# Optimization experiments

Hardware: AMD Instinct MI355X
Metric: run time of the kernel (lower is better)

Reference implementation:

```python
import jax, jax.numpy as jnp
import numpy as np

D_EMB = 1024
N_HEADS = 16
HEAD_SIZE = 64
LN_EPS = 1e-5


def _layernorm(x, g, b):
    mu = jnp.mean(x, axis=-1, keepdims=True)
    var = jnp.var(x, axis=-1, keepdims=True)
    return (x - mu) * jax.lax.rsqrt(var + LN_EPS) * g + b


def setup_inputs() -> dict:
    key = jax.random.key(0)
    ks = jax.random.split(key, 16)
    B, N, D, H, HS = 8, 1024, D_EMB, N_HEADS, HEAD_SIZE
    s_in = 1.0 / np.sqrt(D)
    s_h = 1.0 / np.sqrt(H * HS)
    s_ff = 1.0 / np.sqrt(4 * D)
    return {
        "x": jax.random.normal(ks[0], (B, N, D), jnp.float32),
        # per-head q/k/v projections, stacked over heads: [H, D, HS]
        "Wq": jax.random.normal(ks[1], (H, D, HS), jnp.float32) * s_in,
        "bq": jnp.zeros((H, HS), jnp.float32),
        "Wk": jax.random.normal(ks[2], (H, D, HS), jnp.float32) * s_in,
        "bk": jnp.zeros((H, HS), jnp.float32),
        "Wv": jax.random.normal(ks[3], (H, D, HS), jnp.float32) * s_in,
        "bv": jnp.zeros((H, HS), jnp.float32),
        "Wproj": jax.random.normal(ks[4], (H * HS, D), jnp.float32) * s_h,
        "bproj": jnp.zeros((D,), jnp.float32),
        "W1": jax.random.normal(ks[5], (D, 4 * D), jnp.float32) * s_in,
        "b1": jnp.zeros((4 * D,), jnp.float32),
        "W2": jax.random.normal(ks[6], (4 * D, D), jnp.float32) * s_ff,
        "b2": jnp.zeros((D,), jnp.float32),
        "ln1_g": jnp.ones((D,), jnp.float32),
        "ln1_b": jnp.zeros((D,), jnp.float32),
        "ln2_g": jnp.ones((D,), jnp.float32),
        "ln2_b": jnp.zeros((D,), jnp.float32),
    }


def reference(x, Wq, bq, Wk, bk, Wv, bv, Wproj, bproj, W1, b1, W2, b2,
              ln1_g, ln1_b, ln2_g, ln2_b):
    # --- pre-LN multi-head attention (dropout = identity in eval) ---
    h = _layernorm(x, ln1_g, ln1_b)                    # [B, N, D]
    q = jnp.einsum('bnd,hds->bhns', h, Wq) + bq[None, :, None, :]
    k = jnp.einsum('bnd,hds->bhns', h, Wk) + bk[None, :, None, :]
    v = jnp.einsum('bnd,hds->bhns', h, Wv) + bv[None, :, None, :]
    scale = 1.0 / jnp.sqrt(jnp.float32(HEAD_SIZE))
    wei = jnp.einsum('bhns,bhms->bhnm', q, k) * scale  # [B, H, N, N]
    wei = jax.nn.softmax(wei, axis=-1)
    attn = jnp.einsum('bhnm,bhms->bhns', wei, v)       # [B, H, N, HS]
    B, H, N, HS = attn.shape
    attn = attn.transpose(0, 2, 1, 3).reshape(B, N, H * HS)  # concat heads
    x = x + attn @ Wproj + bproj
    # --- pre-LN feed-forward with LeakyReLU ---
    h2 = _layernorm(x, ln2_g, ln2_b)
    ff = jax.nn.leaky_relu(h2 @ W1 + b1, negative_slope=0.01) @ W2 + b2
    return x + ff
```

## Files before the change

kernel.cpp:

```cpp
#include <hip/hip_runtime.h>
#include <cstdint>
#include <cstddef>

typedef unsigned short u16;
typedef __attribute__((ext_vector_type(4))) float f32x4;
typedef __attribute__((ext_vector_type(8))) short s16x8;

#define D_EMB 1024
#define NSEQ 1024
#define NB 8
#define NH 16
#define HS 64
#define DFF 4096
#define MTOT (NB*NSEQ)

__device__ __forceinline__ u16 f2bf(float f){
  unsigned u = __float_as_uint(f);
  u += 0x7FFFu + ((u >> 16) & 1u);
  return (u16)(u >> 16);
}

__global__ void transpose_cvt(const float* __restrict__ in, u16* __restrict__ out,
                              int R, int C, size_t inStride, size_t outStride){
  __shared__ float t[32][33];
  const float* ip = in + (size_t)blockIdx.z * inStride;
  u16* op = out + (size_t)blockIdx.z * outStride;
  int c0 = blockIdx.x * 32, r0 = blockIdx.y * 32;
  int tx = threadIdx.x, ty = threadIdx.y;
#pragma unroll
  for (int j = 0; j < 32; j += 8)
    t[ty + j][tx] = ip[(size_t)(r0 + ty + j) * C + (c0 + tx)];
  __syncthreads();
#pragma unroll
  for (int j = 0; j < 32; j += 8)
    op[(size_t)(c0 + ty + j) * R + (r0 + tx)] = f2bf(t[tx][ty + j]);
}

__global__ __launch_bounds__(256) void ln_kernel(const float* __restrict__ x,
    const float* __restrict__ g, const float* __restrict__ bb, u16* __restrict__ out){
  int row = blockIdx.x;
  const float* xr = x + (size_t)row * D_EMB;
  int c = threadIdx.x * 4;
  f32x4 v = *(const f32x4*)(xr + c);
  float s1 = v[0] + v[1] + v[2] + v[3];
  float s2 = v[0]*v[0] + v[1]*v[1] + v[2]*v[2] + v[3]*v[3];
#pragma unroll
  for (int m = 32; m > 0; m >>= 1){ s1 += __shfl_xor(s1, m); s2 += __shfl_xor(s2, m); }
  __shared__ float ps1[4], ps2[4];
  int w = threadIdx.x >> 6;
  if ((threadIdx.x & 63) == 0){ ps1[w] = s1; ps2[w] = s2; }
  __syncthreads();
  s1 = ps1[0] + ps1[1] + ps1[2] + ps1[3];
  s2 = ps2[0] + ps2[1] + ps2[2] + ps2[3];
  float mu = s1 * (1.f / D_EMB);
  float var = s2 * (1.f / D_EMB) - mu * mu;
  float rs = rsqrtf(var + 1e-5f);
  ushort4 o;
  o.x = f2bf((v[0]-mu)*rs*g[c+0] + bb[c+0]);
  o.y = f2bf((v[1]-mu)*rs*g[c+1] + bb[c+1]);
  o.z = f2bf((v[2]-mu)*rs*g[c+2] + bb[c+2]);
  o.w = f2bf((v[3]-mu)*rs*g[c+3] + bb[c+3]);
  *(ushort4*)(out + (size_t)row * D_EMB + c) = o;
}

#define BM 128
#define BN 128
#define BK 32

__device__ __forceinline__ void gload_lds16(const void* g, void* l){
  __builtin_amdgcn_global_load_lds((const __attribute__((address_space(1))) void*)g,
                                   (__attribute__((address_space(3))) void*)l, 16, 0, 0);
}

template<int MODE>
__global__ __launch_bounds__(256) void gemm_bt(
    const u16* __restrict__ A, const u16* __restrict__ Bt,
    int M, int N, int K,
    const float* __restrict__ bias0, const float* __restrict__ bias1,
    const float* __restrict__ bias2, const float* __restrict__ resid,
    void* __restrict__ o0, void* __restrict__ o1, void* __restrict__ o2)
{
  __shared__ alignas(16) u16 Al[2][BM*BK];
  __shared__ alignas(16) u16 Bl[2][BN*BK];
  const int tid = threadIdx.x;
  const int m0 = blockIdx.x * BM, n0 = blockIdx.y * BN;
  const int wid = tid >> 6, lane = tid & 63;
  const int wm = (wid >> 1) * 64, wn = (wid & 1) * 64;
  const int lr = lane & 15, lg = lane >> 4;

  f32x4 zero = {0.f, 0.f, 0.f, 0.f};
  f32x4 acc[4][4];
#pragma unroll
  for (int i = 0; i < 4; i++)
#pragma unroll
    for (int j = 0; j < 4; j++) acc[i][j] = zero;

  const int nk = K / BK;
  const int arow = tid >> 2, akg = tid & 3;

  auto stage = [&](int bufi, int kt){
    const int k0 = kt * BK;
    const u16* ap = A  + (size_t)(m0 + arow) * K + k0 + akg * 8;
    gload_lds16(ap,                  &Al[bufi][tid * 8]);
    gload_lds16(ap + (size_t)64 * K, &Al[bufi][2048 + tid * 8]);
    const u16* bp = Bt + (size_t)(n0 + arow) * K + k0 + akg * 8;
    gload_lds16(bp,                  &Bl[bufi][tid * 8]);
    gload_lds16(bp + (size_t)64 * K, &Bl[bufi][2048 + tid * 8]);
  };

  stage(0, 0);
  for (int kt = 0; kt < nk; ++kt){
    __syncthreads();
    if (kt + 1 < nk) stage((kt + 1) & 1, kt + 1);
    const int bufi = kt & 1;
    s16x8 af[4], bfr[4];
#pragma unroll
    for (int i = 0; i < 4; i++){
      af[i]  = *(const s16x8*)&Al[bufi][(wm + i*16 + lr) * BK + lg * 8];
      bfr[i] = *(const s16x8*)&Bl[bufi][(wn + i*16 + lr) * BK + lg * 8];
    }
#pragma unroll
    for (int i = 0; i < 4; i++)
#pragma unroll
      for (int j = 0; j < 4; j++)
        acc[i][j] = __builtin_amdgcn_mfma_f32_16x16x32_bf16(af[i], bfr[j], acc[i][j], 0, 0, 0);
  }

#pragma unroll
  for (int fm = 0; fm < 4; fm++){
    const int gmb = m0 + wm + fm * 16 + lg * 4;
#pragma unroll
    for (int fn = 0; fn < 4; fn++){
      const int gn = n0 + wn + fn * 16 + lr;
#pragma unroll
      for (int i = 0; i < 4; i++){
        const int gm = gmb + i;
        float v = acc[fm][fn][i];
        if (MODE == 0){
          const int cls = gn >> 10, nn = gn & 1023;
          if (cls == 0)      ((u16*)o0)[(size_t)gm * D_EMB + nn] = f2bf(v + bias0[nn]);
          else if (cls == 1) ((u16*)o1)[(size_t)gm * D_EMB + nn] = f2bf(v + bias1[nn]);
          else {
            const int hh = nn >> 6, ss = nn & 63, bb = gm >> 10, tt = gm & 1023;
            ((u16*)o2)[(((size_t)(bb * NH + hh)) * HS + ss) * NSEQ + tt] = f2bf(v + bias2[nn]);
          }
        } else if (MODE == 1){
          ((float*)o0)[(size_t)gm * N + gn] = resid[(size_t)gm * N + gn] + v + bias0[gn];
        } else {
          float y = v + bias0[gn];
          y = y > 0.f ? y : 0.01f * y;
          ((u16*)o0)[(size_t)gm * N + gn] = f2bf(y);
        }
      }
    }
  }
}

__global__ __launch_bounds__(256) void attn_kernel(
    const u16* __restrict__ Qb, const u16* __restrict__ Kb, const u16* __restrict__ VT,
    u16* __restrict__ attnC)
{
  const int bid = blockIdx.x;
  const int bh = bid & 127, qt = bid >> 7;
  const int b = bh >> 4, h = bh & 15;
  const int tid = threadIdx.x, w = tid >> 6, lane = tid & 63;
  const int lr = lane & 15, lg = lane >> 4;
  const int q0 = qt * 128 + w * 32;

  __shared__ alignas(16) u16 Kl[2][64*64];
  __shared__ alignas(16) u16 Vl[2][64*64];
  __shared__ alignas(16) u16 Pl[4][32][72];

  const int srow = tid >> 3, scg = tid & 7;
  const u16* kbase = Kb + (size_t)(b * NSEQ) * D_EMB + h * HS;
  const u16* vbase = VT + ((size_t)(b * NH + h)) * HS * NSEQ;

  auto stage = [&](int buf, int kt){
    const int tk = kt * 64;
#pragma unroll
    for (int p = 0; p < 2; ++p){
      const int row = srow + p * 32;
      const int sc = scg ^ (row & 7);
      gload_lds16(kbase + (size_t)(tk + row) * D_EMB + sc * 8, &Kl[buf][(p * 256 + tid) * 8]);
      gload_lds16(vbase + (size_t)row * NSEQ + tk + sc * 8,    &Vl[buf][(p * 256 + tid) * 8]);
    }
  };

  s16x8 aq[2][2];
#pragma unroll
  for (int rb = 0; rb < 2; rb++)
#pragma unroll
    for (int kh = 0; kh < 2; kh++)
      aq[rb][kh] = *(const s16x8*)(Qb + (size_t)(b * NSEQ + q0 + rb * 16 + lr) * D_EMB
                                   + h * HS + kh * 32 + lg * 8);

  float m_i[2][4], l_i[2][4];
  f32x4 zero = {0.f, 0.f, 0.f, 0.f};
  f32x4 ao[2][4];
#pragma unroll
  for (int rb = 0; rb < 2; rb++)
#pragma unroll
    for (int i = 0; i < 4; i++){ m_i[rb][i] = -1e30f; l_i[rb][i] = 0.f; ao[rb][i] = zero; }

  const float scale = 0.125f;
  const int rsw = lr & 7;

  stage(0, 0);
  for (int kt = 0; kt < NSEQ / 64; ++kt){
    __syncthreads();
    if (kt + 1 < NSEQ / 64) stage((kt + 1) & 1, kt + 1);
    const int cur = kt & 1;

    f32x4 sv[2][4];
#pragma unroll
    for (int rb = 0; rb < 2; rb++)
#pragma unroll
      for (int fn = 0; fn < 4; fn++) sv[rb][fn] = zero;
#pragma unroll
    for (int fn = 0; fn < 4; fn++){
      const int krow = fn * 16 + lr;
#pragma unroll
      for (int kh = 0; kh < 2; kh++){
        const int chunk = (kh * 4 + lg) ^ rsw;
        s16x8 kf = *(const s16x8*)&Kl[cur][krow * 64 + chunk * 8];
        sv[0][fn] = __builtin_amdgcn_mfma_f32_16x16x32_bf16(aq[0][kh], kf, sv[0][fn], 0, 0, 0);
        sv[1][fn] = __builtin_amdgcn_mfma_f32_16x16x32_bf16(aq[1][kh], kf, sv[1][fn], 0, 0, 0);
      }
    }

#pragma unroll
    for (int rb = 0; rb < 2; rb++){
      float p[4][4];
#pragma unroll
      for (int i = 0; i < 4; i++){
        float s0 = sv[rb][0][i] * scale, s1 = sv[rb][1][i] * scale;
        float s2 = sv[rb][2][i] * scale, s3 = sv[rb][3][i] * scale;
        float rmax = fmaxf(fmaxf(s0, s1), fmaxf(s2, s3));
#pragma unroll
        for (int mm = 8; mm > 0; mm >>= 1) rmax = fmaxf(rmax, __shfl_xor(rmax, mm));
        float mnew = fmaxf(m_i[rb][i], rmax);
        float fac = __expf(m_i[rb][i] - mnew);
        float p0 = __expf(s0 - mnew), p1 = __expf(s1 - mnew);
        float p2 = __expf(s2 - mnew), p3 = __expf(s3 - mnew);
        p[0][i] = p0; p[1][i] = p1; p[2][i] = p2; p[3][i] = p3;
        float rs = (p0 + p1) + (p2 + p3);
#pragma unroll
        for (int mm = 8; mm > 0; mm >>= 1) rs += __shfl_xor(rs, mm);
        l_i[rb][i] = l_i[rb][i] * fac + rs;
        m_i[rb][i] = mnew;
#pragma unroll
        for (int fn = 0; fn < 4; fn++) ao[rb][fn][i] *= fac;
      }
#pragma unroll
      for (int fn = 0; fn < 4; fn++)
#pragma unroll
        for (int i = 0; i < 4; i++)
          Pl[w][rb * 16 + lg * 4 + i][fn * 16 + lr] = f2bf(p[fn][i]);
    }

    s16x8 vf[4][2];
#pragma unroll
    for (int fn = 0; fn < 4; fn++){
      const int vrow = fn * 16 + lr;
#pragma unroll
      for (int kh = 0; kh < 2; kh++){
        const int chunk = (kh * 4 + lg) ^ rsw;
        vf[fn][kh] = *(const s16x8*)&Vl[cur][vrow * 64 + chunk * 8];
      }
    }
#pragma unroll
    for (int rb = 0; rb < 2; rb++){
      s16x8 pa0 = *(const s16x8*)&Pl[w][rb * 16 + lr][lg * 8];
      s16x8 pa1 = *(const s16x8*)&Pl[w][rb * 16 + lr][32 + lg * 8];
#pragma unroll
      for (int fn = 0; fn < 4; fn++){
        ao[rb][fn] = __builtin_amdgcn_mfma_f32_16x16x32_bf16(pa0, vf[fn][0], ao[rb][fn], 0, 0, 0);
        ao[rb][fn] = __builtin_amdgcn_mfma_f32_16x16x32_bf16(pa1, vf[fn][1], ao[rb][fn], 0, 0, 0);
      }
    }
  }

#pragma unroll
  for (int rb = 0; rb < 2; rb++)
#pragma unroll
    for (int fn = 0; fn < 4; fn++)
#pragma unroll
      for (int i = 0; i < 4; i++){
        float v = ao[rb][fn][i] / l_i[rb][i];
        attnC[(size_t)(b * NSEQ + q0 + rb * 16 + lg * 4 + i) * D_EMB + h * HS + fn * 16 + lr] = f2bf(v);
      }
}

extern "C" void kernel_launch(void* const* d_in, const int* in_sizes, int n_in,
                              void* d_out, int out_size, void* d_ws, size_t ws_size,
                              hipStream_t stream)
{
  const float* x    = (const float*)d_in[0];
  const float* Wq   = (const float*)d_in[1];
  const float* bq   = (const float*)d_in[2];
  const float* Wk   = (const float*)d_in[3];
  const float* bk   = (const float*)d_in[4];
  const float* Wv   = (const float*)d_in[5];
  const float* bv   = (const float*)d_in[6];
  const float* Wp   = (const float*)d_in[7];
  const float* bp   = (const float*)d_in[8];
  const float* W1   = (const float*)d_in[9];
  const float* b1   = (const float*)d_in[10];
  const float* W2   = (const float*)d_in[11];
  const float* b2   = (const float*)d_in[12];
  const float* ln1g = (const float*)d_in[13];
  const float* ln1b = (const float*)d_in[14];
  const float* ln2g = (const float*)d_in[15];
  const float* ln2b = (const float*)d_in[16];
  float* out = (float*)d_out;

  char* ws = (char*)d_ws;
  size_t off = 0;
  auto mk = [&](size_t bytes)->void*{ void* p = ws + off; off += (bytes + 255) & ~(size_t)255; return p; };
  u16*  h1    = (u16*) mk((size_t)MTOT * D_EMB * 2);
  u16*  Qb    = (u16*) mk((size_t)MTOT * D_EMB * 2);
  u16*  Kb    = (u16*) mk((size_t)MTOT * D_EMB * 2);
  u16*  VTb   = (u16*) mk((size_t)MTOT * D_EMB * 2);
  u16*  attnC = (u16*) mk((size_t)MTOT * D_EMB * 2);
  float* x1   = (float*)mk((size_t)MTOT * D_EMB * 4);
  u16*  h2    = (u16*) mk((size_t)MTOT * D_EMB * 2);
  u16*  ffb   = (u16*) mk((size_t)MTOT * DFF * 2);
  u16*  WqkvT = (u16*) mk((size_t)3 * D_EMB * D_EMB * 2);
  u16*  WpT   = (u16*) mk((size_t)D_EMB * D_EMB * 2);
  u16*  W1T   = (u16*) mk((size_t)D_EMB * DFF * 2);
  u16*  W2T   = (u16*) mk((size_t)D_EMB * DFF * 2);

  dim3 tb(32, 8, 1);
  transpose_cvt<<<dim3(HS/32, D_EMB/32, NH), tb, 0, stream>>>(Wq, WqkvT,                         D_EMB, HS, (size_t)D_EMB*HS, (size_t)HS*D_EMB);
  transpose_cvt<<<dim3(HS/32, D_EMB/32, NH), tb, 0, stream>>>(Wk, WqkvT + (size_t)D_EMB*D_EMB,   D_EMB, HS, (size_t)D_EMB*HS, (size_t)HS*D_EMB);
  transpose_cvt<<<dim3(HS/32, D_EMB/32, NH), tb, 0, stream>>>(Wv, WqkvT + (size_t)2*D_EMB*D_EMB, D_EMB, HS, (size_t)D_EMB*HS, (size_t)HS*D_EMB);
  transpose_cvt<<<dim3(D_EMB/32, D_EMB/32, 1), tb, 0, stream>>>(Wp, WpT,  D_EMB, D_EMB, 0, 0);
  transpose_cvt<<<dim3(DFF/32,  D_EMB/32, 1), tb, 0, stream>>>(W1, W1T,  D_EMB, DFF,   0, 0);
  transpose_cvt<<<dim3(D_EMB/32, DFF/32,  1), tb, 0, stream>>>(W2, W2T,  DFF,   D_EMB, 0, 0);

  ln_kernel<<<MTOT, 256, 0, stream>>>(x, ln1g, ln1b, h1);

  gemm_bt<0><<<dim3(MTOT/BM, (3*D_EMB)/BN), 256, 0, stream>>>(h1, WqkvT, MTOT, 3*D_EMB, D_EMB,
      bq, bk, bv, nullptr, Qb, Kb, VTb);

  attn_kernel<<<NB*NH*(NSEQ/128), 256, 0, stream>>>(Qb, Kb, VTb, attnC);

  gemm_bt<1><<<dim3(MTOT/BM, D_EMB/BN), 256, 0, stream>>>(attnC, WpT, MTOT, D_EMB, D_EMB,
      bp, nullptr, nullptr, x, x1, nullptr, nullptr);

  ln_kernel<<<MTOT, 256, 0, stream>>>(x1, ln2g, ln2b, h2);

  gemm_bt<2><<<dim3(MTOT/BM, DFF/BN), 256, 0, stream>>>(h2, W1T, MTOT, DFF, D_EMB,
      b1, nullptr, nullptr, nullptr, ffb, nullptr, nullptr);

  gemm_bt<1><<<dim3(MTOT/BM, D_EMB/BN), 256, 0, stream>>>(ffb, W2T, MTOT, D_EMB, DFF,
      b2, nullptr, nullptr, x1, out, nullptr, nullptr);
}
```

Before: 470.9 us.

## Add 256-row 8-wave GEMM with swizzled LDS, XCD remap and split-phase pipelining

Adds a new GEMM kernel with 256xBN tiles, 512 threads, and BK=64 split into two 32-wide halves. It double-buffers through dynamic LDS with an XOR swizzle, interleaves loads with MFMA using barriers and setprio, and remaps block IDs across XCDs. The aim is more data reuse per tile and better overlap of global loads with matrix math for the QKV, projection, FF1 and FF2 GEMMs. The cost is large LDS use (up to 128KB), which limits occupancy, plus a fallback to the old kernel if the shared-memory attribute cannot be set.

```diff
diff --git a/kernel.cpp b/kernel.cpp
--- a/kernel.cpp
+++ b/kernel.cpp
@@ -18,6 +18,11 @@
   unsigned u = __float_as_uint(f);
   u += 0x7FFFu + ((u >> 16) & 1u);
   return (u16)(u >> 16);
+}
+
+__device__ __forceinline__ void gload_lds16(const void* g, void* l){
+  __builtin_amdgcn_global_load_lds((const __attribute__((address_space(1))) void*)g,
+                                   (__attribute__((address_space(3))) void*)l, 16, 0, 0);
 }
 
 __global__ void transpose_cvt(const float* __restrict__ in, u16* __restrict__ out,
@@ -63,15 +68,155 @@
   *(ushort4*)(out + (size_t)row * D_EMB + c) = o;
 }
 
+template<int MODE, int BNT>
+__global__ __launch_bounds__(512) void gemm256(
+    const u16* __restrict__ A, const u16* __restrict__ Bt,
+    int M, int N, int K,
+    const float* __restrict__ bias0, const float* __restrict__ bias1,
+    const float* __restrict__ bias2, const float* __restrict__ resid,
+    void* __restrict__ o0, void* __restrict__ o1, void* __restrict__ o2)
+{
+  constexpr int BMT = 256;
+  constexpr int WCN = BNT/64, WRN = 8/WCN;
+  constexpr int WROWS = BMT/WRN;
+  constexpr int RF = WROWS/16, RH = RF/2;
+  constexpr int ALD = 2, BLD = (BNT*32)/(512*8);
+  constexpr int AHALF = BMT*32, BHALF = BNT*32;
+  extern __shared__ u16 lds[];
+  u16* const Ab = lds;
+  u16* const Bb = lds + 4*AHALF;
+
+  const int tid = threadIdx.x;
+  const int wid = tid>>6, lane = tid&63, lr = lane&15, lg = lane>>4;
+  const int wr = wid/WCN, wc = wid%WCN;
+
+  const int gx = gridDim.x;
+  const int nwg = gx * gridDim.y;
+  const int bid = blockIdx.x + blockIdx.y*gx;
+  const int wg = (bid&7)*(nwg>>3) + (bid>>3);
+  const int m0 = (wg % gx) * BMT;
+  const int n0 = (wg / gx) * BNT;
+
+  const int nkt = K/64;
+  const int srow = tid>>2;
+  const int sl = (tid&3) ^ ((tid>>2)&3);
+
+  auto stageA = [&](int nb, int kt1, int kh){
+    const u16* src = A + (size_t)m0 * K + (size_t)kt1*64 + kh*32 + sl*8;
+    u16* dst = Ab + (nb*2 + kh)*AHALF + tid*8;
+#pragma unroll
+    for (int r = 0; r < ALD; ++r)
+      gload_lds16(src + (size_t)(r*128 + srow)*K, dst + r*4096);
+  };
+  auto stageB = [&](int nb, int kt1, int kh){
+    const u16* src = Bt + (size_t)n0 * K + (size_t)kt1*64 + kh*32 + sl*8;
+    u16* dst = Bb + (nb*2 + kh)*BHALF + tid*8;
+#pragma unroll
+    for (int r = 0; r < BLD; ++r)
+      gload_lds16(src + (size_t)(r*128 + srow)*K, dst + r*4096);
+  };
+  auto rdA = [&](int cur, int kh, int fm) -> s16x8 {
+    const int row = wr*WROWS + fm*16 + lr;
+    return *(const s16x8*)&Ab[(cur*2+kh)*AHALF + row*32 + ((lg ^ (row&3))<<3)];
+  };
+  auto rdB = [&](int cur, int kh, int fn) -> s16x8 {
+    const int row = wc*64 + fn*16 + lr;
+    return *(const s16x8*)&Bb[(cur*2+kh)*BHALF + row*32 + ((lg ^ (row&3))<<3)];
+  };
+  auto waitv = [&](){
+    if constexpr (ALD + BLD == 4) asm volatile("s_waitcnt vmcnt(4)" ::: "memory");
+    else                          asm volatile("s_waitcnt vmcnt(3)" ::: "memory");
+  };
+
+  f32x4 acc[RF][4];
+#pragma unroll
+  for (int i = 0; i < RF; i++)
+#pragma unroll
+    for (int j = 0; j < 4; j++) acc[i][j] = {0.f,0.f,0.f,0.f};
+
+  stageA(0,0,0); stageB(0,0,0); stageA(0,0,1); stageB(0,0,1);
+  waitv();
+  __builtin_amdgcn_s_barrier();
+
+  s16x8 bf[4];
+  for (int kt = 0; kt < nkt; ++kt){
+    const int cur = kt&1, nb = cur^1;
+    const bool st = (kt+1 < nkt);
+#pragma unroll
+    for (int kh = 0; kh < 2; ++kh){
+      s16x8 af[RH];
+#pragma unroll
+      for (int j = 0; j < RH; ++j) af[j] = rdA(cur, kh, j);
+#pragma unroll
+      for (int fn = 0; fn < 4; ++fn) bf[fn] = rdB(cur, kh, fn);
+      if (st){ if (kh == 0) stageA(nb, kt+1, 0); else stageA(nb, kt+1, 1); }
+      __builtin_amdgcn_s_barrier();
+      asm volatile("s_waitcnt lgkmcnt(0)" ::: "memory");
+      __builtin_amdgcn_sched_barrier(0);
+      __builtin_amdgcn_s_setprio(1);
+#pragma unroll
+      for (int j = 0; j < RH; ++j)
+#pragma unroll
+        for (int fn = 0; fn < 4; ++fn)
+          acc[j][fn] = __builtin_amdgcn_mfma_f32_16x16x32_bf16(af[j], bf[fn], acc[j][fn], 0, 0, 0);
+      __builtin_amdgcn_s_setprio(0);
+      __builtin_amdgcn_s_barrier();
+#pragma unroll
+      for (int j = 0; j < RH; ++j) af[j] = rdA(cur, kh, RH + j);
+      if (st){ if (kh == 0) stageB(nb, kt+1, 0); else stageB(nb, kt+1, 1); }
+      __builtin_amdgcn_s_barrier();
+      asm volatile("s_waitcnt lgkmcnt(0)" ::: "memory");
+      __builtin_amdgcn_sched_barrier(0);
+      __builtin_amdgcn_s_setprio(1);
+#pragma unroll
+      for (int j = 0; j < RH; ++j)
+#pragma unroll
+        for (int fn = 0; fn < 4; ++fn)
+          acc[RH+j][fn] = __builtin_amdgcn_mfma_f32_16x16x32_bf16(af[j], bf[fn], acc[RH+j][fn], 0, 0, 0);
+      __builtin_amdgcn_s_setprio(0);
+      if (kh == 0){
+        if (st) waitv();
+        else    asm volatile("s_waitcnt vmcnt(0)" ::: "memory");
+      } else {
+        if (st) waitv();
+      }
+      __builtin_amdgcn_s_barrier();
+    }
+  }
+
+#pragma unroll
+  for (int fm = 0; fm < RF; fm++){
+    const int gmb = m0 + wr*WROWS + fm*16 + lg*4;
+#pragma unroll
+    for (int fn = 0; fn < 4; fn++){
+      const int gn = n0 + wc*64 + fn*16 + lr;
+#pragma unroll
+      for (int i = 0; i < 4; i++){
+        const int gm = gmb + i;
+        float v = acc[fm][fn][i];
+        if (MODE == 0){
+          const int cls = gn >> 10, nn = gn & 1023;
+          if (cls == 0)      ((u16*)o0)[(size_t)gm * D_EMB + nn] = f2bf(v + bias0[nn]);
+          else if (cls == 1) ((u16*)o1)[(size_t)gm * D_EMB + nn] = f2bf(v + bias1[nn]);
+          else {
+            const int hh = nn >> 6, ss = nn & 63, bb = gm >> 10, tt = gm & 1023;
+            ((u16*)o2)[(((size_t)(bb * NH + hh)) * HS + ss) * NSEQ + tt] = f2bf(v + bias2[nn]);
+          }
+        } else if (MODE == 1){
+          ((float*)o0)[(size_t)gm * N + gn] = resid[(size_t)gm * N + gn] + v + bias0[gn];
+        } else {
+          float y = v + bias0[gn];
+          y = y > 0.f ? y : 0.01f * y;
+          ((u16*)o0)[(size_t)gm * N + gn] = f2bf(y);
+        }
+      }
+    }
+  }
+}
+
 #define BM 128
 #define BN 128
 #define BK 32
-
-__device__ __forceinline__ void gload_lds16(const void* g, void* l){
-  __builtin_amdgcn_global_load_lds((const __attribute__((address_space(1))) void*)g,
-                                   (__attribute__((address_space(3))) void*)l, 16, 0, 0);
-}
-
 template<int MODE>
 __global__ __launch_bounds__(256) void gemm_bt(
     const u16* __restrict__ A, const u16* __restrict__ Bt,
@@ -88,12 +233,11 @@
   const int wm = (wid >> 1) * 64, wn = (wid & 1) * 64;
   const int lr = lane & 15, lg = lane >> 4;
 
-  f32x4 zero = {0.f, 0.f, 0.f, 0.f};
   f32x4 acc[4][4];
 #pragma unroll
   for (int i = 0; i < 4; i++)
 #pragma unroll
-    for (int j = 0; j < 4; j++) acc[i][j] = zero;
+    for (int j = 0; j < 4; j++) acc[i][j] = {0.f,0.f,0.f,0.f};
 
   const int nk = K / BK;
   const int arow = tid >> 2, akg = tid & 3;
@@ -340,19 +484,35 @@
 
   ln_kernel<<<MTOT, 256, 0, stream>>>(x, ln1g, ln1b, h1);
 
-  gemm_bt<0><<<dim3(MTOT/BM, (3*D_EMB)/BN), 256, 0, stream>>>(h1, WqkvT, MTOT, 3*D_EMB, D_EMB,
-      bq, bk, bv, nullptr, Qb, Kb, VTb);
-
-  attn_kernel<<<NB*NH*(NSEQ/128), 256, 0, stream>>>(Qb, Kb, VTb, attnC);
-
-  gemm_bt<1><<<dim3(MTOT/BM, D_EMB/BN), 256, 0, stream>>>(attnC, WpT, MTOT, D_EMB, D_EMB,
-      bp, nullptr, nullptr, x, x1, nullptr, nullptr);
-
-  ln_kernel<<<MTOT, 256, 0, stream>>>(x1, ln2g, ln2b, h2);
-
-  gemm_bt<2><<<dim3(MTOT/BM, DFF/BN), 256, 0, stream>>>(h2, W1T, MTOT, DFF, D_EMB,
-      b1, nullptr, nullptr, nullptr, ffb, nullptr, nullptr);
-
-  gemm_bt<1><<<dim3(MTOT/BM, D_EMB/BN), 256, 0, stream>>>(ffb, W2T, MTOT, D_EMB, DFF,
-      b2, nullptr, nullptr, x1, out, nullptr, nullptr);
-}
+  bool big = true;
+  big &= hipFuncSetAttribute(reinterpret_cast<const void*>(&gemm256<0,256>),
+                             hipFuncAttributeMaxDynamicSharedMemorySize, 131072) == hipSuccess;
+  big &= hipFuncSetAttribute(reinterpret_cast<const void*>(&gemm256<2,256>),
+                             hipFuncAttributeMaxDynamicSharedMemorySize, 131072) == hipSuccess;
+  big &= hipFuncSetAttribute(reinterpret_cast<const void*>(&gemm256<1,128>),
+                             hipFuncAttributeMaxDynamicSharedMemorySize, 98304) == hipSuccess;
+
+  if (big){
+    gemm256<0,256><<<dim3(MTOT/256, 3*D_EMB/256), 512, 131072, stream>>>(h1, WqkvT, MTOT, 3*D_EMB, D_EMB,
+        bq, bk, bv, nullptr, Qb, Kb, VTb);
+    attn_kernel<<<NB*NH*(NSEQ/128), 256, 0, stream>>>(Qb, Kb, VTb, attnC);
+    gemm256<1,128><<<dim3(MTOT/256, D_EMB/128), 512, 98304, stream>>>(attnC, WpT, MTOT, D_EMB, D_EMB,
+        bp, nullptr, nullptr, x, x1, nullptr, nullptr);
+    ln_kernel<<<MTOT, 256, 0, stream>>>(x1, ln2g, ln2b, h2);
+    gemm256<2,256><<<dim3(MTOT/256, DFF/256), 512, 131072, stream>>>(h2, W1T, MTOT, DFF, D_EMB,
+        b1, nullptr, nullptr, nullptr, ffb, nullptr, nullptr);
+    gemm256<1,128><<<dim3(MTOT/256, D_EMB/128), 512, 98304, stream>>>(ffb, W2T, MTOT, D_EMB, DFF,
+        b2, nullptr, nullptr, x1, out, nullptr, nullptr);
+  } else {
+    gemm_bt<0><<<dim3(MTOT/BM, (3*D_EMB)/BN), 256, 0, stream>>>(h1, WqkvT, MTOT, 3*D_EMB, D_EMB,
+        bq, bk, bv, nullptr, Qb, Kb, VTb);
+    attn_kernel<<<NB*NH*(NSEQ/128), 256, 0, stream>>>(Qb, Kb, VTb, attnC);
+    gemm_bt<1><<<dim3(MTOT/BM, D_EMB/BN), 256, 0, stream>>>(attnC, WpT, MTOT, D_EMB, D_EMB,
+        bp, nullptr, nullptr, x, x1, nullptr, nullptr);
+    ln_kernel<<<MTOT, 256, 0, stream>>>(x1, ln2g, ln2b, h2);
+    gemm_bt<2><<<dim3(MTOT/BM, DFF/BN), 256, 0, stream>>>(h2, W1T, MTOT, DFF, D_EMB,
+        b1, nullptr, nullptr, nullptr, ffb, nullptr, nullptr);
+    gemm_bt<1><<<dim3(MTOT/BM, D_EMB/BN), 256, 0, stream>>>(ffb, W2T, MTOT, D_EMB, DFF,
+        b2, nullptr, nullptr, x1, out, nullptr, nullptr);
+  }
+}
```

Result: slower. 503.8 us (+7.0%).

## Templatize GEMM with larger tiles, XCD-aware block remap and LDS swizzle

Applied to the files above, without the earlier changes.

Replaces the fixed 128x128 GEMM with a templated kernel using 128x256 (512 threads) or 64x256 tiles per projection. It remaps block IDs across the eight XCDs so neighbouring tiles share L2, and swizzles the K-chunk placement in LDS to avoid bank conflicts on fragment reads. The aim is more data reuse per tile, better cache locality and fewer LDS stalls. The cost is higher register and LDS pressure per block, and fewer blocks for the smaller-N GEMMs.

```diff
diff --git a/kernel.cpp b/kernel.cpp
--- a/kernel.cpp
+++ b/kernel.cpp
@@ -18,6 +18,11 @@
   unsigned u = __float_as_uint(f);
   u += 0x7FFFu + ((u >> 16) & 1u);
   return (u16)(u >> 16);
+}
+
+__device__ __forceinline__ void gload_lds16(const void* g, void* l){
+  __builtin_amdgcn_global_load_lds((const __attribute__((address_space(1))) void*)g,
+                                   (__attribute__((address_space(3))) void*)l, 16, 0, 0);
 }
 
 __global__ void transpose_cvt(const float* __restrict__ in, u16* __restrict__ out,
@@ -63,75 +68,81 @@
   *(ushort4*)(out + (size_t)row * D_EMB + c) = o;
 }
 
-#define BM 128
-#define BN 128
-#define BK 32
-
-__device__ __forceinline__ void gload_lds16(const void* g, void* l){
-  __builtin_amdgcn_global_load_lds((const __attribute__((address_space(1))) void*)g,
-                                   (__attribute__((address_space(3))) void*)l, 16, 0, 0);
-}
-
-template<int MODE>
-__global__ __launch_bounds__(256) void gemm_bt(
+template<int MODE, int BMT, int BNT, int NTHR>
+__global__ __launch_bounds__(NTHR) void gemm2ph(
     const u16* __restrict__ A, const u16* __restrict__ Bt,
     int M, int N, int K,
     const float* __restrict__ bias0, const float* __restrict__ bias1,
     const float* __restrict__ bias2, const float* __restrict__ resid,
     void* __restrict__ o0, void* __restrict__ o1, void* __restrict__ o2)
 {
-  __shared__ alignas(16) u16 Al[2][BM*BK];
-  __shared__ alignas(16) u16 Bl[2][BN*BK];
+  constexpr int NWAVE = NTHR/64;
+  constexpr int WCN = BNT/64, WRN = NWAVE/WCN;
+  static_assert(BMT/WRN == 64, "wave tile is 64x64");
+  constexpr int RPP = NTHR/4;
+  constexpr int ALD = (BMT*32)/(NTHR*8);
+  constexpr int BLD = (BNT*32)/(NTHR*8);
+  __shared__ alignas(16) u16 Al[2][BMT*32];
+  __shared__ alignas(16) u16 Bl[2][BNT*32];
+
   const int tid = threadIdx.x;
-  const int m0 = blockIdx.x * BM, n0 = blockIdx.y * BN;
-  const int wid = tid >> 6, lane = tid & 63;
-  const int wm = (wid >> 1) * 64, wn = (wid & 1) * 64;
-  const int lr = lane & 15, lg = lane >> 4;
-
-  f32x4 zero = {0.f, 0.f, 0.f, 0.f};
+  const int wid = tid>>6, lane = tid&63, lr = lane&15, lg = lane>>4;
+  const int wr = wid/WCN, wc = wid%WCN;
+
+  const int gx = gridDim.x;
+  const int nwg = gx * gridDim.y;
+  const int bid = blockIdx.x + blockIdx.y*gx;
+  const int wg = (bid&7)*(nwg>>3) + (bid>>3);
+  const int m0 = (wg % gx) * BMT;
+  const int n0 = (wg / gx) * BNT;
+
+  const int srow = tid>>2;
+  const int scs = (((tid&3) - ((srow>>1)&3)) & 3) * 8;
+
+  auto stage = [&](int buf, int kt){
+    const u16* asrc = A + (size_t)(m0 + srow)*K + kt*32 + scs;
+#pragma unroll
+    for (int r = 0; r < ALD; ++r)
+      gload_lds16(asrc + (size_t)(r*RPP)*K, &Al[buf][r*(NTHR*8) + tid*8]);
+    const u16* bsrc = Bt + (size_t)(n0 + srow)*K + kt*32 + scs;
+#pragma unroll
+    for (int r = 0; r < BLD; ++r)
+      gload_lds16(bsrc + (size_t)(r*RPP)*K, &Bl[buf][r*(NTHR*8) + tid*8]);
+  };
+
   f32x4 acc[4][4];
 #pragma unroll
   for (int i = 0; i < 4; i++)
 #pragma unroll
-    for (int j = 0; j < 4; j++) acc[i][j] = zero;
-
-  const int nk = K / BK;
-  const int arow = tid >> 2, akg = tid & 3;
-
-  auto stage = [&](int bufi, int kt){
-    const int k0 = kt * BK;
-    const u16* ap = A  + (size_t)(m0 + arow) * K + k0 + akg * 8;
-    gload_lds16(ap,                  &Al[bufi][tid * 8]);
-    gload_lds16(ap + (size_t)64 * K, &Al[bufi][2048 + tid * 8]);
-    const u16* bp = Bt + (size_t)(n0 + arow) * K + k0 + akg * 8;
-    gload_lds16(bp,                  &Bl[bufi][tid * 8]);
-    gload_lds16(bp + (size_t)64 * K, &Bl[bufi][2048 + tid * 8]);
-  };
-
+    for (int j = 0; j < 4; j++) acc[i][j] = {0.f,0.f,0.f,0.f};
+
+  const int nk = K/32;
   stage(0, 0);
   for (int kt = 0; kt < nk; ++kt){
     __syncthreads();
-    if (kt + 1 < nk) stage((kt + 1) & 1, kt + 1);
-    const int bufi = kt & 1;
-    s16x8 af[4], bfr[4];
+    if (kt + 1 < nk) stage((kt+1)&1, kt+1);
+    const int buf = kt & 1;
+    s16x8 af[4], bf[4];
 #pragma unroll
     for (int i = 0; i < 4; i++){
-      af[i]  = *(const s16x8*)&Al[bufi][(wm + i*16 + lr) * BK + lg * 8];
-      bfr[i] = *(const s16x8*)&Bl[bufi][(wn + i*16 + lr) * BK + lg * 8];
+      const int ar = wr*64 + i*16 + lr;
+      af[i] = *(const s16x8*)&Al[buf][ar*32 + (((lg + (ar>>1)) & 3)<<3)];
+      const int br = wc*64 + i*16 + lr;
+      bf[i] = *(const s16x8*)&Bl[buf][br*32 + (((lg + (br>>1)) & 3)<<3)];
     }
 #pragma unroll
     for (int i = 0; i < 4; i++)
 #pragma unroll
       for (int j = 0; j < 4; j++)
-        acc[i][j] = __builtin_amdgcn_mfma_f32_16x16x32_bf16(af[i], bfr[j], acc[i][j], 0, 0, 0);
+        acc[i][j] = __builtin_amdgcn_mfma_f32_16x16x32_bf16(af[i], bf[j], acc[i][j], 0, 0, 0);
   }
 
 #pragma unroll
   for (int fm = 0; fm < 4; fm++){
-    const int gmb = m0 + wm + fm * 16 + lg * 4;
+    const int gmb = m0 + wr*64 + fm*16 + lg*4;
 #pragma unroll
     for (int fn = 0; fn < 4; fn++){
-      const int gn = n0 + wn + fn * 16 + lr;
+      const int gn = n0 + wc*64 + fn*16 + lr;
 #pragma unroll
       for (int i = 0; i < 4; i++){
         const int gm = gmb + i;
@@ -340,19 +351,19 @@
 
   ln_kernel<<<MTOT, 256, 0, stream>>>(x, ln1g, ln1b, h1);
 
-  gemm_bt<0><<<dim3(MTOT/BM, (3*D_EMB)/BN), 256, 0, stream>>>(h1, WqkvT, MTOT, 3*D_EMB, D_EMB,
-      bq, bk, bv, nullptr, Qb, Kb, VTb);
+  gemm2ph<0,128,256,512><<<dim3(MTOT/128, 3*D_EMB/256), 512, 0, stream>>>(
+      h1, WqkvT, MTOT, 3*D_EMB, D_EMB, bq, bk, bv, nullptr, Qb, Kb, VTb);
 
   attn_kernel<<<NB*NH*(NSEQ/128), 256, 0, stream>>>(Qb, Kb, VTb, attnC);
 
-  gemm_bt<1><<<dim3(MTOT/BM, D_EMB/BN), 256, 0, stream>>>(attnC, WpT, MTOT, D_EMB, D_EMB,
-      bp, nullptr, nullptr, x, x1, nullptr, nullptr);
+  gemm2ph<1,64,256,256><<<dim3(MTOT/64, D_EMB/256), 256, 0, stream>>>(
+      attnC, WpT, MTOT, D_EMB, D_EMB, bp, nullptr, nullptr, x, x1, nullptr, nullptr);
 
   ln_kernel<<<MTOT, 256, 0, stream>>>(x1, ln2g, ln2b, h2);
 
-  gemm_bt<2><<<dim3(MTOT/BM, DFF/BN), 256, 0, stream>>>(h2, W1T, MTOT, DFF, D_EMB,
-      b1, nullptr, nullptr, nullptr, ffb, nullptr, nullptr);
-
-  gemm_bt<1><<<dim3(MTOT/BM, D_EMB/BN), 256, 0, stream>>>(ffb, W2T, MTOT, D_EMB, DFF,
-      b2, nullptr, nullptr, x1, out, nullptr, nullptr);
-}
+  gemm2ph<2,128,256,512><<<dim3(MTOT/128, DFF/256), 512, 0, stream>>>(
+      h2, W1T, MTOT, DFF, D_EMB, b1, nullptr, nullptr, nullptr, ffb, nullptr, nullptr);
+
+  gemm2ph<1,64,256,256><<<dim3(MTOT/64, D_EMB/256), 256, 0, stream>>>(
+      ffb, W2T, MTOT, D_EMB, DFF, b2, nullptr, nullptr, x1, out, nullptr, nullptr);
+}
```

Result: slower. 486.0 us (+3.2%).
